# Optimization experiments

Measured on AMD Instinct MI355X. Metric: run time of the kernel, lower is better.

## Reference

```python
import jax, jax.numpy as jnp
import numpy as np
from jax import lax

V, D, H, L, K = 50257, 1024, 2048, 6, 3
B, S = 4, 2048
EPS = 1.1920929e-07  # torch.finfo(float32).eps (torch RMSNorm default eps=None)


def rmsnorm(x, w):
    return x * lax.rsqrt(jnp.mean(x * x, axis=-1, keepdims=True) + EPS) * w


def depthwise_conv(x, w, b):
    # x: (B,S,D), w: (D,1,K) depthwise kernel, padding='same' as in torch Conv1d
    y = lax.conv_general_dilated(x.transpose(0, 2, 1), w, (1,), 'SAME',
                                 dimension_numbers=('NCH', 'OIH', 'NCH'),
                                 feature_group_count=x.shape[-1])
    return y.transpose(0, 2, 1) + b


def mingru(x, h0, wz, bz, wh, bh, wo, bo):
    # minGRU: z=sigmoid(Wz x), h_tilde=Wh x, h_t=(1-z_t)h_{t-1}+z_t h_tilde_t (parallel scan)
    z = jax.nn.sigmoid(jnp.einsum('bsd,hd->bsh', x, wz) + bz)
    htil = jnp.einsum('bsd,hd->bsh', x, wh) + bh
    a, bc = 1.0 - z, z * htil

    def comb(c1, c2):
        a1, b1 = c1
        a2, b2 = c2
        return a1 * a2, a2 * b1 + b2

    A, Bc = lax.associative_scan(comb, (a, bc), axis=1)
    h = A * h0[:, None, :] + Bc                      # (B,S,H)
    out = jnp.einsum('bsh,dh->bsd', h, wo) + bo      # project back to model dim
    return out, h[:, -1]


def setup_inputs():
    key = jax.random.key(0)
    ks = jax.random.split(key, 16)
    sc = 0.02
    p = {}
    p['x'] = jax.random.randint(ks[0], (B, S), 0, V)
    p['h_prev'] = jax.random.normal(ks[1], (B, L, H), jnp.float32)
    p['emb'] = jax.random.normal(ks[2], (V, D), jnp.float32) * sc
    p['conv_dw_w'] = jax.random.normal(ks[3], (L, D, 1, K), jnp.float32) * sc
    p['conv_dw_b'] = jnp.zeros((L, D), jnp.float32)
    p['conv_pw_w'] = jax.random.normal(ks[4], (L, D, D), jnp.float32) * sc
    p['conv_pw_b'] = jnp.zeros((L, D), jnp.float32)
    p['n1_w'] = jnp.ones((L, D), jnp.float32)
    p['wz'] = jax.random.normal(ks[5], (L, H, D), jnp.float32) * sc
    p['bz'] = jnp.zeros((L, H), jnp.float32)
    p['wh'] = jax.random.normal(ks[6], (L, H, D), jnp.float32) * sc
    p['bh'] = jnp.zeros((L, H), jnp.float32)
    p['wo'] = jax.random.normal(ks[7], (L, D, H), jnp.float32) * sc
    p['bo'] = jnp.zeros((L, D), jnp.float32)
    p['n2_w'] = jnp.ones((L, D), jnp.float32)
    p['f1_w'] = jax.random.normal(ks[8], (L, H, D), jnp.float32) * sc
    p['f1_b'] = jnp.zeros((L, H), jnp.float32)
    p['f2_w'] = jax.random.normal(ks[9], (L, D, H), jnp.float32) * sc
    p['f2_b'] = jnp.zeros((L, D), jnp.float32)
    p['norm_w'] = jnp.ones((D,), jnp.float32)
    p['out_w'] = jax.random.normal(ks[10], (H, D), jnp.float32) * sc
    p['out_b'] = jnp.zeros((H,), jnp.float32)
    return p


def reference(x, h_prev, emb, conv_dw_w, conv_dw_b, conv_pw_w, conv_pw_b, n1_w,
              wz, bz, wh, bh, wo, bo, n2_w, f1_w, f1_b, f2_w, f2_b,
              norm_w, out_w, out_b):
    xe = emb[x]                                      # (B,S,D)
    h_next = []
    for l in range(L):
        c = depthwise_conv(xe, conv_dw_w[l], conv_dw_b[l])
        c = jnp.einsum('bsd,ed->bse', c, conv_pw_w[l]) + conv_pw_b[l]  # 1x1 conv
        xe = c + xe
        g, hl = mingru(rmsnorm(xe, n1_w[l]), h_prev[:, l],
                       wz[l], bz[l], wh[l], bh[l], wo[l], bo[l])
        xe = g + xe
        f = rmsnorm(xe, n2_w[l])
        f = jnp.einsum('bsd,hd->bsh', f, f1_w[l]) + f1_b[l]
        f = jax.nn.gelu(f, approximate=False)
        f = jnp.einsum('bsh,dh->bsd', f, f2_w[l]) + f2_b[l]
        xe = f + xe
        h_next.append(hl)
    out = jnp.einsum('bsd,hd->bsh', rmsnorm(xe, norm_w), out_w) + out_b
    return out, jnp.stack(h_next, axis=1)             # (B,S,H), (B,L,H)
```

## Files before the change

kernel.cpp:

```cpp
#include <hip/hip_runtime.h>

typedef __bf16 bf16x8 __attribute__((ext_vector_type(8)));
typedef float f32x4 __attribute__((ext_vector_type(4)));

#define DEVI __device__ __forceinline__

namespace {
constexpr int cB = 4, cS = 2048, cD = 1024, cH = 2048, cL = 6;
constexpr int cM = cB * cS;
constexpr float cEPS = 1.1920929e-07f;
constexpr int NCH = 16, CHS = cS / NCH;
}

DEVI unsigned short f2bf(float f) {
  union { float f; unsigned u; } c; c.f = f;
  const unsigned u = c.u;
  return (unsigned short)((u + 0x7fffu + ((u >> 16) & 1u)) >> 16);
}
DEVI float bf2f(unsigned short h) {
  union { unsigned u; float f; } c; c.u = ((unsigned)h) << 16;
  return c.f;
}

DEVI void gld16(const void* g, void* l) {
  __builtin_amdgcn_global_load_lds(
      (__attribute__((address_space(1))) void*)g,
      (__attribute__((address_space(3))) void*)l, 16, 0, 0);
}

union F4 { float4 v; float a[4]; };

__global__ __launch_bounds__(256) void embed_k(const int* __restrict__ x,
    const float* __restrict__ emb, float* __restrict__ xe) {
  const int bs = blockIdx.x;
  const int idx = x[bs];
  const int t = threadIdx.x;
  *(float4*)&xe[(size_t)bs * cD + t * 4] =
      *(const float4*)&emb[(size_t)idx * cD + t * 4];
}

__global__ __launch_bounds__(256) void dwconv_k(const float* __restrict__ xe,
    const float* __restrict__ w, const float* __restrict__ bias,
    unsigned short* __restrict__ out) {
  const int bs = blockIdx.x;
  const int s = bs & (cS - 1);
  const int t = threadIdx.x;
  const int d = t * 4;
  const size_t base = (size_t)bs * cD + d;
  F4 x0, xm, xp, vb;
  x0.v = *(const float4*)&xe[base];
  xm.v = make_float4(0.f, 0.f, 0.f, 0.f);
  xp.v = make_float4(0.f, 0.f, 0.f, 0.f);
  if (s > 0) xm.v = *(const float4*)&xe[base - cD];
  if (s < cS - 1) xp.v = *(const float4*)&xe[base + cD];
  vb.v = *(const float4*)&bias[d];
  unsigned short o[4];
#pragma unroll
  for (int j = 0; j < 4; ++j) {
    const float w0 = w[(d + j) * 3 + 0];
    const float w1 = w[(d + j) * 3 + 1];
    const float w2 = w[(d + j) * 3 + 2];
    o[j] = f2bf(xm.a[j] * w0 + x0.a[j] * w1 + xp.a[j] * w2 + vb.a[j]);
  }
  *(ushort4*)&out[base] = make_ushort4(o[0], o[1], o[2], o[3]);
}

__global__ __launch_bounds__(256) void rmsnorm_k(const float* __restrict__ x,
    const float* __restrict__ w, unsigned short* __restrict__ o) {
  const int row = blockIdx.x;
  const int t = threadIdx.x;
  const size_t base = (size_t)row * cD + t * 4;
  F4 v; v.v = *(const float4*)&x[base];
  float ss = v.a[0]*v.a[0] + v.a[1]*v.a[1] + v.a[2]*v.a[2] + v.a[3]*v.a[3];
#pragma unroll
  for (int off = 32; off > 0; off >>= 1) ss += __shfl_down(ss, off, 64);
  __shared__ float red[4];
  if ((t & 63) == 0) red[t >> 6] = ss;
  __syncthreads();
  const float scale = rsqrtf((red[0]+red[1]+red[2]+red[3]) * (1.f/cD) + cEPS);
  F4 wv; wv.v = *(const float4*)&w[t * 4];
  *(ushort4*)&o[base] = make_ushort4(
      f2bf(v.a[0]*scale*wv.a[0]), f2bf(v.a[1]*scale*wv.a[1]),
      f2bf(v.a[2]*scale*wv.a[2]), f2bf(v.a[3]*scale*wv.a[3]));
}

__global__ __launch_bounds__(256) void wcvt_k(
    const float* __restrict__ s0, unsigned short* __restrict__ d0,
    const float* __restrict__ s1, unsigned short* __restrict__ d1,
    const float* __restrict__ s2, unsigned short* __restrict__ d2,
    const float* __restrict__ s3, unsigned short* __restrict__ d3,
    const float* __restrict__ s4, unsigned short* __restrict__ d4) {
  constexpr size_t nPW = (size_t)cL * cD * cD;
  constexpr size_t nHD = (size_t)cL * cD * cH;
  constexpr size_t b0 = nPW, b1 = b0 + nHD, b2 = b1 + nHD, b3 = b2 + nHD;
  constexpr size_t total = b3 + (size_t)cH * cD;
  const size_t i = ((size_t)blockIdx.x * 256 + threadIdx.x) * 4;
  if (i >= total) return;
  const float* s; unsigned short* d; size_t off;
  if (i < b0)      { s = s0; d = d0; off = i; }
  else if (i < b1) { s = s1; d = d1; off = i - b0; }
  else if (i < b2) { s = s2; d = d2; off = i - b1; }
  else if (i < b3) { s = s3; d = d3; off = i - b2; }
  else             { s = s4; d = d4; off = i - b3; }
  F4 v; v.v = *(const float4*)&s[off];
  *(ushort4*)&d[off] = make_ushort4(f2bf(v.a[0]), f2bf(v.a[1]),
                                    f2bf(v.a[2]), f2bf(v.a[3]));
}

__global__ __launch_bounds__(256) void cvti2_k(const float* __restrict__ wz,
    const float* __restrict__ wh, unsigned short* __restrict__ d) {
  const size_t i = ((size_t)blockIdx.x * 256 + threadIdx.x) * 4;
  const int l = (int)(i >> 21);
  const int r = (int)((i >> 10) & (cH - 1));
  const int c = (int)(i & (cD - 1));
  F4 a, b; a.v = *(const float4*)&wz[i]; b.v = *(const float4*)&wh[i];
  const size_t dz = (((size_t)l * 2 * cH) + 2 * r) * cD + c;
  *(ushort4*)&d[dz] = make_ushort4(f2bf(a.a[0]), f2bf(a.a[1]),
                                   f2bf(a.a[2]), f2bf(a.a[3]));
  *(ushort4*)&d[dz + cD] = make_ushort4(f2bf(b.a[0]), f2bf(b.a[1]),
                                        f2bf(b.a[2]), f2bf(b.a[3]));
}

__global__ __launch_bounds__(256) void biasi2_k(const float* __restrict__ bz,
    const float* __restrict__ bh, float* __restrict__ d) {
  const int i = blockIdx.x * 256 + threadIdx.x;
  const int l = i >> 11, h = i & (cH - 1);
  d[((size_t)l * 2 * cH) + 2 * h]     = bz[i];
  d[((size_t)l * 2 * cH) + 2 * h + 1] = bh[i];
}

template<int N, int K, int EPI>
__global__ __launch_bounds__(256) void gemm_bt(
    const unsigned short* __restrict__ A, const unsigned short* __restrict__ W,
    const float* __restrict__ bias, float* __restrict__ Cf,
    unsigned short* __restrict__ Cb) {
  __shared__ unsigned short As[128 * 32];
  __shared__ unsigned short Bs[128 * 32];
  const int t = threadIdx.x;
  const int lane = t & 63;
  const int wave = t >> 6;
  const int m0 = blockIdx.x * 128;
  const int n0 = blockIdx.y * 128;
  const int wm = (wave >> 1) * 64;
  const int wn = (wave & 1) * 64;
  const int fr = lane & 15;
  const int fk = ((lane >> 4) * 8) ^ (((lane >> 1) & 3) << 3);

  const int arow = t >> 2;
  const int acol = (((t & 3) ^ ((t >> 3) & 3)) * 8);
  const unsigned short* gA = A + (size_t)(m0 + arow) * K + acol;
  const unsigned short* gB = W + (size_t)(n0 + arow) * K + acol;
  unsigned short* lA = As + wave * 512;
  unsigned short* lB = Bs + wave * 512;

  f32x4 acc[4][4] = {};
  for (int k0 = 0; k0 < K; k0 += 32) {
    gld16(gA + k0, lA);
    gld16(gA + k0 + (size_t)64 * K, lA + 2048);
    gld16(gB + k0, lB);
    gld16(gB + k0 + (size_t)64 * K, lB + 2048);
    __syncthreads();
    bf16x8 fa[4], fb[4];
#pragma unroll
    for (int i = 0; i < 4; ++i) {
      fa[i] = *(const bf16x8*)&As[(wm + i * 16 + fr) * 32 + fk];
      fb[i] = *(const bf16x8*)&Bs[(wn + i * 16 + fr) * 32 + fk];
    }
#pragma unroll
    for (int i = 0; i < 4; ++i)
#pragma unroll
      for (int j = 0; j < 4; ++j)
        acc[i][j] = __builtin_amdgcn_mfma_f32_16x16x32_bf16(
            fa[i], fb[j], acc[i][j], 0, 0, 0);
    __syncthreads();
  }

  const int r0 = m0 + wm + ((lane >> 4) << 2);
  const int c0 = n0 + wn + fr;
#pragma unroll
  for (int i = 0; i < 4; ++i)
#pragma unroll
    for (int j = 0; j < 4; ++j) {
      const int col = c0 + j * 16;
      const float bv = bias[col];
#pragma unroll
      for (int r = 0; r < 4; ++r) {
        const size_t idx = (size_t)(r0 + i * 16 + r) * N + col;
        const float v = acc[i][j][r] + bv;
        if constexpr (EPI == 1) {
          Cf[idx] += v;
        } else {
          Cf[idx] = v;
        }
      }
    }
}

#define RDA(BUF, MH)                                                        \
  _Pragma("unroll") for (int mf = 0; mf < 4; ++mf)                          \
  _Pragma("unroll") for (int kk = 0; kk < 2; ++kk)                          \
      a[mf * 2 + kk] = *(const bf16x8*)&lds[(BUF)*16384 + aB + (MH)*4096 +  \
                                            mf * 1024 + ((kk) ? ck1 : ck0)];

#define RDB0(BUF)                                                           \
  _Pragma("unroll") for (int q = 0; q < 2; ++q)                             \
  _Pragma("unroll") for (int kk = 0; kk < 2; ++kk)                          \
      b[0][q * 2 + kk] = *(const bf16x8*)&lds[(BUF)*16384 + bB + q * 1024 + \
                                              ((kk) ? ck1 : ck0)];

#define RDB1(BUF)                                                           \
  _Pragma("unroll") for (int q = 2; q < 4; ++q)                             \
  _Pragma("unroll") for (int kk = 0; kk < 2; ++kk)                          \
      b[1][(q & 1) * 2 + kk] =                                              \
          *(const bf16x8*)&lds[(BUF)*16384 + bB + q * 1024 +                \
                               ((kk) ? ck1 : ck0)];

#define MMQ(MH, NH)                                                         \
  _Pragma("unroll") for (int mf = 0; mf < 4; ++mf)                          \
  _Pragma("unroll") for (int nf = 0; nf < 2; ++nf)                          \
  _Pragma("unroll") for (int kk = 0; kk < 2; ++kk)                          \
      acc[(MH)*4 + mf][(NH)*2 + nf] = __builtin_amdgcn_mfma_f32_16x16x32_bf16( \
          a[mf * 2 + kk], b[NH][nf * 2 + kk], acc[(MH)*4 + mf][(NH)*2 + nf],  \
          0, 0, 0);

#define PH_SYNC()                                                           \
  __builtin_amdgcn_s_barrier();                                             \
  asm volatile("s_waitcnt lgkmcnt(0)" ::: "memory");                        \
  __builtin_amdgcn_sched_barrier(0);                                        \
  __builtin_amdgcn_s_setprio(1)

#define PH_END()                                                            \
  __builtin_amdgcn_s_setprio(0);                                            \
  __builtin_amdgcn_s_barrier()

#define TILE_PHASES(TI, BUF, OBUF, S1, S2, VM)                              \
  {                                                                         \
    RDA(BUF, 0); RDB0(BUF);                                                 \
    if (S1) { stA((TI) + 1, 1, ldsA(OBUF, 1)); }                            \
    asm volatile("s_waitcnt lgkmcnt(8)" ::: "memory");                      \
    PH_SYNC(); MMQ(0, 0); PH_END();                                         \
    RDB1(BUF);                                                              \
    PH_SYNC(); MMQ(0, 1); PH_END();                                         \
    RDA(BUF, 1);                                                            \
    if (S2) { stB((TI) + 2, 0, ldsB(BUF, 0)); }                             \
    PH_SYNC(); MMQ(1, 1); PH_END();                                         \
    if (S2) { stB((TI) + 2, 1, ldsB(BUF, 1)); stA((TI) + 2, 0, ldsA(BUF, 0)); } \
    if (VM == 6) { asm volatile("s_waitcnt vmcnt(6)" ::: "memory"); }       \
    else         { asm volatile("s_waitcnt vmcnt(0)" ::: "memory"); }       \
    PH_SYNC(); MMQ(1, 0); PH_END();                                         \
  }

template<int N, int K, int EPI>
__global__ __launch_bounds__(512, 2) void gemm8p(
    const unsigned short* __restrict__ A,
    const unsigned short* __restrict__ W0,
    const float* __restrict__ bias0,
    float* __restrict__ Cf, unsigned short* __restrict__ Cb,
    unsigned short* __restrict__ Cb2,
    float* __restrict__ Ac, float* __restrict__ Bc) {
  static_assert(K % 128 == 0, "NT must be even");
  constexpr int NT = K / 64;
  __shared__ unsigned short lds[65536];
  const int t = threadIdx.x;
  const int lane = t & 63;
  const int wave = t >> 6;
  const int wr = wave >> 2;
  const int wc = wave & 3;
  const int m0 = blockIdx.x * 256;
  const int n0 = blockIdx.y * 256;

  const int srow = t >> 3;
  const int scol = (((t & 7) ^ ((t >> 3) & 7)) * 8);
  const unsigned short* gA = A  + (size_t)(m0 + srow) * K + scol;
  const unsigned short* gB = W0 + (size_t)(n0 + srow) * K + scol;
  const int ldsw = wave * 512;

  auto ldsA = [&](int buf, int h) -> unsigned short* {
    return (unsigned short*)&lds[buf * 16384 + h * 8192 + ldsw];
  };
  auto ldsB = [&](int buf, int h) -> unsigned short* {
    return (unsigned short*)&lds[32768 + buf * 16384 + h * 8192 + ldsw];
  };
  auto stA = [&](int tile, int h, unsigned short* dst) {
    const unsigned short* s = gA + (size_t)(h * 128) * K + tile * 64;
    gld16(s, dst);
    gld16(s + (size_t)64 * K, dst + 4096);
  };
  auto stB = [&](int tile, int h, unsigned short* dst) {
    const unsigned short* s = gB + (size_t)(h * 128) * K + tile * 64;
    gld16(s, dst);
    gld16(s + (size_t)64 * K, dst + 4096);
  };

  const int swz = (lane & 7) << 3;
  const int ck0 = (((lane >> 4) * 8)) ^ swz;
  const int ck1 = (32 + ((lane >> 4) * 8)) ^ swz;
  const int aB = wr * 8192 + (lane & 15) * 64;
  const int bB = 32768 + (wc >> 1) * 8192 + (wc & 1) * 4096 + (lane & 15) * 64;

  bf16x8 a[8];
  bf16x8 b[2][4];
  f32x4 acc[8][4] = {};

  stA(0, 0, ldsA(0, 0)); stA(0, 1, ldsA(0, 1));
  stB(0, 0, ldsB(0, 0)); stB(0, 1, ldsB(0, 1));
  stA(1, 0, ldsA(1, 0));
  stB(1, 0, ldsB(1, 0)); stB(1, 1, ldsB(1, 1));
  asm volatile("s_waitcnt vmcnt(6)" ::: "memory");
  __builtin_amdgcn_s_barrier();

  for (int tp = 0; tp < NT / 2 - 1; ++tp) {
    const int t0 = 2 * tp;
    TILE_PHASES(t0, 0, 1, 1, 1, 6);
    TILE_PHASES(t0 + 1, 1, 0, 1, 1, 6);
  }
  TILE_PHASES(NT - 2, 0, 1, 1, 0, 0);
  TILE_PHASES(NT - 1, 1, 0, 0, 0, 0);

  const int r0l = wr * 128 + ((lane >> 4) << 2);
  const int c0l = wc * 64 + (lane & 15);
  if constexpr (EPI == 0) {
    const int r0 = m0 + r0l;
    const int c0 = n0 + c0l;
#pragma unroll
    for (int mfg = 0; mfg < 8; ++mfg)
#pragma unroll
      for (int nfg = 0; nfg < 4; ++nfg) {
        const int col = c0 + nfg * 16;
        const float bv = bias0[col];
#pragma unroll
        for (int r = 0; r < 4; ++r)
          Cf[(size_t)(r0 + mfg * 16 + r) * N + col] = acc[mfg][nfg][r] + bv;
      }
  } else {
    const bool isz = ((lane & 1) == 0);
#pragma unroll
    for (int mfg = 0; mfg < 8; ++mfg)
#pragma unroll
      for (int nfg = 0; nfg < 4; ++nfg) {
        const int col = c0l + nfg * 16;
        const float bv = bias0[n0 + col];
#pragma unroll
        for (int r = 0; r < 4; ++r) {
          const float v = acc[mfg][nfg][r] + bv;
          unsigned short o;
          if constexpr (EPI == 4) {
            o = f2bf(0.5f * v * (1.f + erff(v * 0.70710678118654752f)));
          } else {
            o = isz ? f2bf(1.f / (1.f + __expf(-v))) : f2bf(v);
          }
          const int rr = r0l + mfg * 16 + r;
          lds[rr * 256 + (col ^ (((rr >> 2) & 3) << 4))] = o;
        }
      }
    __syncthreads();
    if constexpr (EPI == 4) {
#pragma unroll
      for (int it = 0; it < 16; ++it) {
        const int flat = it * 512 + t;
        const int row = flat >> 5;
        const int ch = flat & 31;
        const float4 v = *(const float4*)&lds[row * 256 +
                                              ((ch * 8) ^ (((row >> 2) & 3) << 4))];
        *(float4*)&Cb[(size_t)(m0 + row) * N + n0 + ch * 8] = v;
      }
    } else {
#pragma unroll
      for (int it = 0; it < 16; ++it) {
        const int flat = it * 512 + t;
        const int row = flat >> 5;
        const int ch = flat & 31;
        union { float4 v; unsigned u[4]; } q;
        q.v = *(const float4*)&lds[row * 256 +
                                   ((ch * 8) ^ (((row >> 2) & 3) << 4))];
        const ushort4 zz = make_ushort4(q.u[0] & 0xffff, q.u[1] & 0xffff,
                                        q.u[2] & 0xffff, q.u[3] & 0xffff);
        const ushort4 hh = make_ushort4(q.u[0] >> 16, q.u[1] >> 16,
                                        q.u[2] >> 16, q.u[3] >> 16);
        const size_t o = (size_t)(m0 + row) * (N / 2) + (n0 >> 1) + ch * 4;
        *(ushort4*)&Cb[o]  = zz;
        *(ushort4*)&Cb2[o] = hh;
      }
      if (t < 256) {
        const int lc = t >> 7;
        const int lh = t & 127;
        float av = 1.f, bv = 0.f;
        const int s0 = lc * 128;
#pragma unroll 4
        for (int s = 0; s < CHS; ++s) {
          const int sr = s0 + s;
          const int c = (2 * lh) ^ (((sr >> 2) & 3) << 4);
          const unsigned w2 = *(const unsigned*)&lds[sr * 256 + c];
          const float zv = bf2f((unsigned short)(w2 & 0xffff));
          const float hv = bf2f((unsigned short)(w2 >> 16));
          const float aa = 1.f - zv;
          bv = aa * bv + zv * hv;
          av *= aa;
        }
        const int bidx = m0 / cS;
        const int ck = ((m0 & (cS - 1)) >> 7) + lc;
        const int hg = (n0 >> 1) + lh;
        const size_t so = ((size_t)bidx * NCH + ck) * cH + hg;
        Ac[so] = av;
        Bc[so] = bv;
      }
    }
  }
}

__global__ __launch_bounds__(256) void scan23_k(const unsigned short* __restrict__ z,
    unsigned short* __restrict__ ht, const float* __restrict__ Ac,
    const float* __restrict__ Bc, const float* __restrict__ h_prev,
    float* __restrict__ hn, int l) {
  const int tid = blockIdx.x * 256 + threadIdx.x;
  const int hq = (tid & (cH / 4 - 1)) * 4;
  const int ck = (tid / (cH / 4)) & (NCH - 1);
  const int b = tid / ((cH / 4) * NCH);
  const size_t hoff = ((size_t)b * cL + l) * cH + hq;
  F4 h0; h0.v = *(const float4*)&h_prev[hoff];
  float r[4] = {h0.a[0], h0.a[1], h0.a[2], h0.a[3]};
  for (int c = 0; c < ck; ++c) {
    const size_t so = ((size_t)b * NCH + c) * cH + hq;
    F4 av, bv;
    av.v = *(const float4*)&Ac[so];
    bv.v = *(const float4*)&Bc[so];
#pragma unroll
    for (int j = 0; j < 4; ++j) r[j] = av.a[j] * r[j] + bv.a[j];
  }
  const size_t base = ((size_t)b * cS + (size_t)ck * CHS) * cH + hq;
#pragma unroll 4
  for (int s = 0; s < CHS; ++s) {
    const ushort4 zz = *(const ushort4*)&z[base + (size_t)s * cH];
    const ushort4 hh = *(const ushort4*)&ht[base + (size_t)s * cH];
    const float zf[4] = {bf2f(zz.x), bf2f(zz.y), bf2f(zz.z), bf2f(zz.w)};
    const float hf[4] = {bf2f(hh.x), bf2f(hh.y), bf2f(hh.z), bf2f(hh.w)};
#pragma unroll
    for (int j = 0; j < 4; ++j) r[j] = (1.f - zf[j]) * r[j] + zf[j] * hf[j];
    *(ushort4*)&ht[base + (size_t)s * cH] =
        make_ushort4(f2bf(r[0]), f2bf(r[1]), f2bf(r[2]), f2bf(r[3]));
  }
  if (ck == NCH - 1)
    *(float4*)&hn[hoff] = make_float4(r[0], r[1], r[2], r[3]);
}

extern "C" void kernel_launch(void* const* d_in, const int* in_sizes, int n_in,
                              void* d_out, int out_size, void* d_ws, size_t ws_size,
                              hipStream_t stream) {
  (void)in_sizes; (void)n_in; (void)out_size; (void)ws_size;
  const int*   x      = (const int*)d_in[0];
  const float* h_prev = (const float*)d_in[1];
  const float* emb    = (const float*)d_in[2];
  const float* cdw_w  = (const float*)d_in[3];
  const float* cdw_b  = (const float*)d_in[4];
  const float* cpw_w  = (const float*)d_in[5];
  const float* cpw_b  = (const float*)d_in[6];
  const float* n1w    = (const float*)d_in[7];
  const float* wzp    = (const float*)d_in[8];
  const float* bzp    = (const float*)d_in[9];
  const float* whp    = (const float*)d_in[10];
  const float* bhp    = (const float*)d_in[11];
  const float* wop    = (const float*)d_in[12];
  const float* bop    = (const float*)d_in[13];
  const float* n2w    = (const float*)d_in[14];
  const float* f1wp   = (const float*)d_in[15];
  const float* f1bp   = (const float*)d_in[16];
  const float* f2wp   = (const float*)d_in[17];
  const float* f2bp   = (const float*)d_in[18];
  const float* nw     = (const float*)d_in[19];
  const float* owp    = (const float*)d_in[20];
  const float* obp    = (const float*)d_in[21];

  float* out_main = (float*)d_out;
  float* out_hn   = out_main + (size_t)cM * cH;

  char* p = (char*)d_ws;
  auto alloc = [&](size_t bytes) {
    char* r = p; p += (bytes + 255) & ~(size_t)255; return r;
  };
  float*          xe = (float*)alloc((size_t)cM * cD * 4);
  unsigned short* xn = (unsigned short*)alloc((size_t)cM * cD * 2);
  unsigned short* zb = (unsigned short*)alloc((size_t)cM * cH * 2);
  unsigned short* hb = (unsigned short*)alloc((size_t)cM * cH * 2);
  float* Ac = (float*)alloc((size_t)cB * NCH * cH * 4);
  float* Bc = (float*)alloc((size_t)cB * NCH * cH * 4);
  unsigned short* w_pw = (unsigned short*)alloc((size_t)cL * cD * cD * 2);
  unsigned short* w_zh = (unsigned short*)alloc((size_t)cL * 2 * cH * cD * 2);
  float*          bzh  = (float*)alloc((size_t)cL * 2 * cH * 4);
  unsigned short* w_o  = (unsigned short*)alloc((size_t)cL * cD * cH * 2);
  unsigned short* w_f1 = (unsigned short*)alloc((size_t)cL * cH * cD * 2);
  unsigned short* w_f2 = (unsigned short*)alloc((size_t)cL * cD * cH * 2);
  unsigned short* w_ow = (unsigned short*)alloc((size_t)cH * cD * 2);

  {
    constexpr size_t total = (size_t)cL * cD * cD + 3 * (size_t)cL * cD * cH +
                             (size_t)cH * cD;
    wcvt_k<<<dim3((unsigned)(total / 1024)), 256, 0, stream>>>(
        cpw_w, w_pw, wop, w_o, f1wp, w_f1, f2wp, w_f2, owp, w_ow);
    cvti2_k<<<dim3(cL * cH * cD / 1024), 256, 0, stream>>>(wzp, whp, w_zh);
    biasi2_k<<<dim3(cL * cH / 256), 256, 0, stream>>>(bzp, bhp, bzh);
  }

  embed_k<<<cM, 256, 0, stream>>>(x, emb, xe);

  for (int l = 0; l < cL; ++l) {
    const size_t oDD = (size_t)l * cD * cD, oHD = (size_t)l * cH * cD;

    dwconv_k<<<cM, 256, 0, stream>>>(xe, cdw_w + (size_t)l * cD * 3,
                                     cdw_b + (size_t)l * cD, xn);
    gemm_bt<cD, cD, 1><<<dim3(cM / 128, cD / 128), 256, 0, stream>>>(
        xn, w_pw + oDD, cpw_b + (size_t)l * cD, xe, nullptr);

    rmsnorm_k<<<cM, 256, 0, stream>>>(xe, n1w + (size_t)l * cD, xn);
    gemm8p<2 * cH, cD, 6><<<dim3(cM / 256, 2 * cH / 256), 512, 0, stream>>>(
        xn, w_zh + (size_t)l * 2 * cH * cD, bzh + (size_t)l * 2 * cH,
        nullptr, zb, hb, Ac, Bc);
    scan23_k<<<cB * NCH * (cH / 4) / 256, 256, 0, stream>>>(zb, hb, Ac, Bc,
                                                            h_prev, out_hn, l);
    gemm_bt<cD, cH, 1><<<dim3(cM / 128, cD / 128), 256, 0, stream>>>(
        hb, w_o + oHD, bop + (size_t)l * cD, xe, nullptr);

    rmsnorm_k<<<cM, 256, 0, stream>>>(xe, n2w + (size_t)l * cD, xn);
    gemm8p<cH, cD, 4><<<dim3(cM / 256, cH / 256), 512, 0, stream>>>(
        xn, w_f1 + oHD, f1bp + (size_t)l * cH, nullptr, zb, nullptr,
        nullptr, nullptr);
    gemm_bt<cD, cH, 1><<<dim3(cM / 128, cD / 128), 256, 0, stream>>>(
        zb, w_f2 + oHD, f2bp + (size_t)l * cD, xe, nullptr);
  }

  rmsnorm_k<<<cM, 256, 0, stream>>>(xe, nw, xn);
  gemm8p<cH, cD, 0><<<dim3(cM / 256, cH / 256), 512, 0, stream>>>(
      xn, w_ow, obp, out_main, nullptr, nullptr, nullptr, nullptr);
}
```

Measured before the change: 2.317 ms.

## Replace simple residual GEMMs with pipelined 256x128 eight-wave MFMA kernel

The three N=1024 residual-add GEMMs (pointwise conv, minGRU output projection, FFN down projection) move from a single-buffered 128x128 kernel with two barriers per K step to a new 512-thread 256x128 kernel. The new kernel uses double-buffered LDS with async prefetch two tiles ahead and phased barriers with s_setprio, mirroring the existing gemm8p schedule. The goal is to hide global load latency and raise MFMA utilisation. In exchange it uses more LDS per block (96KB) and yields half as many blocks (256) per GEMM, which could underfill the GPU.

```diff
diff --git a/kernel.cpp b/kernel.cpp
--- a/kernel.cpp
+++ b/kernel.cpp
@@ -129,100 +129,6 @@
   d[((size_t)l * 2 * cH) + 2 * h + 1] = bh[i];
 }
 
-template<int N, int K, int EPI>
-__global__ __launch_bounds__(256) void gemm_bt(
-    const unsigned short* __restrict__ A, const unsigned short* __restrict__ W,
-    const float* __restrict__ bias, float* __restrict__ Cf,
-    unsigned short* __restrict__ Cb) {
-  __shared__ unsigned short As[128 * 32];
-  __shared__ unsigned short Bs[128 * 32];
-  const int t = threadIdx.x;
-  const int lane = t & 63;
-  const int wave = t >> 6;
-  const int m0 = blockIdx.x * 128;
-  const int n0 = blockIdx.y * 128;
-  const int wm = (wave >> 1) * 64;
-  const int wn = (wave & 1) * 64;
-  const int fr = lane & 15;
-  const int fk = ((lane >> 4) * 8) ^ (((lane >> 1) & 3) << 3);
-
-  const int arow = t >> 2;
-  const int acol = (((t & 3) ^ ((t >> 3) & 3)) * 8);
-  const unsigned short* gA = A + (size_t)(m0 + arow) * K + acol;
-  const unsigned short* gB = W + (size_t)(n0 + arow) * K + acol;
-  unsigned short* lA = As + wave * 512;
-  unsigned short* lB = Bs + wave * 512;
-
-  f32x4 acc[4][4] = {};
-  for (int k0 = 0; k0 < K; k0 += 32) {
-    gld16(gA + k0, lA);
-    gld16(gA + k0 + (size_t)64 * K, lA + 2048);
-    gld16(gB + k0, lB);
-    gld16(gB + k0 + (size_t)64 * K, lB + 2048);
-    __syncthreads();
-    bf16x8 fa[4], fb[4];
-#pragma unroll
-    for (int i = 0; i < 4; ++i) {
-      fa[i] = *(const bf16x8*)&As[(wm + i * 16 + fr) * 32 + fk];
-      fb[i] = *(const bf16x8*)&Bs[(wn + i * 16 + fr) * 32 + fk];
-    }
-#pragma unroll
-    for (int i = 0; i < 4; ++i)
-#pragma unroll
-      for (int j = 0; j < 4; ++j)
-        acc[i][j] = __builtin_amdgcn_mfma_f32_16x16x32_bf16(
-            fa[i], fb[j], acc[i][j], 0, 0, 0);
-    __syncthreads();
-  }
-
-  const int r0 = m0 + wm + ((lane >> 4) << 2);
-  const int c0 = n0 + wn + fr;
-#pragma unroll
-  for (int i = 0; i < 4; ++i)
-#pragma unroll
-    for (int j = 0; j < 4; ++j) {
-      const int col = c0 + j * 16;
-      const float bv = bias[col];
-#pragma unroll
-      for (int r = 0; r < 4; ++r) {
-        const size_t idx = (size_t)(r0 + i * 16 + r) * N + col;
-        const float v = acc[i][j][r] + bv;
-        if constexpr (EPI == 1) {
-          Cf[idx] += v;
-        } else {
-          Cf[idx] = v;
-        }
-      }
-    }
-}
-
-#define RDA(BUF, MH)                                                        \
-  _Pragma("unroll") for (int mf = 0; mf < 4; ++mf)                          \
-  _Pragma("unroll") for (int kk = 0; kk < 2; ++kk)                          \
-      a[mf * 2 + kk] = *(const bf16x8*)&lds[(BUF)*16384 + aB + (MH)*4096 +  \
-                                            mf * 1024 + ((kk) ? ck1 : ck0)];
-
-#define RDB0(BUF)                                                           \
-  _Pragma("unroll") for (int q = 0; q < 2; ++q)                             \
-  _Pragma("unroll") for (int kk = 0; kk < 2; ++kk)                          \
-      b[0][q * 2 + kk] = *(const bf16x8*)&lds[(BUF)*16384 + bB + q * 1024 + \
-                                              ((kk) ? ck1 : ck0)];
-
-#define RDB1(BUF)                                                           \
-  _Pragma("unroll") for (int q = 2; q < 4; ++q)                             \
-  _Pragma("unroll") for (int kk = 0; kk < 2; ++kk)                          \
-      b[1][(q & 1) * 2 + kk] =                                              \
-          *(const bf16x8*)&lds[(BUF)*16384 + bB + q * 1024 +                \
-                               ((kk) ? ck1 : ck0)];
-
-#define MMQ(MH, NH)                                                         \
-  _Pragma("unroll") for (int mf = 0; mf < 4; ++mf)                          \
-  _Pragma("unroll") for (int nf = 0; nf < 2; ++nf)                          \
-  _Pragma("unroll") for (int kk = 0; kk < 2; ++kk)                          \
-      acc[(MH)*4 + mf][(NH)*2 + nf] = __builtin_amdgcn_mfma_f32_16x16x32_bf16( \
-          a[mf * 2 + kk], b[NH][nf * 2 + kk], acc[(MH)*4 + mf][(NH)*2 + nf],  \
-          0, 0, 0);
-
 #define PH_SYNC()                                                           \
   __builtin_amdgcn_s_barrier();                                             \
   asm volatile("s_waitcnt lgkmcnt(0)" ::: "memory");                        \
@@ -232,6 +138,144 @@
 #define PH_END()                                                            \
   __builtin_amdgcn_s_setprio(0);                                            \
   __builtin_amdgcn_s_barrier()
+
+#define RDA_N(BUF, MH)                                                      \
+  _Pragma("unroll") for (int mf = 0; mf < 4; ++mf)                          \
+  _Pragma("unroll") for (int kk = 0; kk < 2; ++kk)                          \
+      a[mf * 2 + kk] = *(const bf16x8*)&lds[(BUF)*16384 + aB + (MH)*4096 +  \
+                                            mf * 1024 + ((kk) ? ck1 : ck0)];
+
+#define RDB_N(BUF, NH)                                                      \
+  _Pragma("unroll") for (int kk = 0; kk < 2; ++kk)                          \
+      b[NH][kk] = *(const bf16x8*)&lds[32768 + (BUF)*8192 + bB +            \
+                                       (NH)*1024 + ((kk) ? ck1 : ck0)];
+
+#define MMQ_N(MH, NH)                                                       \
+  _Pragma("unroll") for (int mf = 0; mf < 4; ++mf)                          \
+  _Pragma("unroll") for (int kk = 0; kk < 2; ++kk)                          \
+      acc[(MH)*4 + mf][NH] = __builtin_amdgcn_mfma_f32_16x16x32_bf16(       \
+          a[mf * 2 + kk], b[NH][kk], acc[(MH)*4 + mf][NH], 0, 0, 0);
+
+#define TILE_N(TI, BUF, OBUF, S1, S2, VM)                                   \
+  {                                                                         \
+    RDA_N(BUF, 0); RDB_N(BUF, 0);                                           \
+    if (S1) { stA((TI) + 1, 1, ldsA(OBUF, 1)); }                            \
+    PH_SYNC(); MMQ_N(0, 0); PH_END();                                       \
+    RDB_N(BUF, 1);                                                          \
+    PH_SYNC(); MMQ_N(0, 1); PH_END();                                       \
+    RDA_N(BUF, 1);                                                          \
+    if (S2) { stB((TI) + 2, ldsB(BUF)); }                                   \
+    PH_SYNC(); MMQ_N(1, 1); PH_END();                                       \
+    if (S2) { stA((TI) + 2, 0, ldsA(BUF, 0)); }                             \
+    if (VM == 4) { asm volatile("s_waitcnt vmcnt(4)" ::: "memory"); }       \
+    else         { asm volatile("s_waitcnt vmcnt(0)" ::: "memory"); }       \
+    PH_SYNC(); MMQ_N(1, 0); PH_END();                                       \
+  }
+
+template<int N, int K>
+__global__ __launch_bounds__(512, 2) void gemm8n(
+    const unsigned short* __restrict__ A,
+    const unsigned short* __restrict__ W,
+    const float* __restrict__ bias, float* __restrict__ Cf) {
+  static_assert(K % 128 == 0, "NT must be even");
+  constexpr int NT = K / 64;
+  __shared__ unsigned short lds[49152];
+  const int t = threadIdx.x;
+  const int lane = t & 63;
+  const int wave = t >> 6;
+  const int wr = wave >> 2;
+  const int wc = wave & 3;
+  const int m0 = blockIdx.x * 256;
+  const int n0 = blockIdx.y * 128;
+
+  const int srow = t >> 3;
+  const int scol = (((t & 7) ^ ((t >> 3) & 7)) * 8);
+  const unsigned short* gA = A + (size_t)(m0 + srow) * K + scol;
+  const unsigned short* gB = W + (size_t)(n0 + srow) * K + scol;
+  const int ldsw = wave * 512;
+
+  auto ldsA = [&](int buf, int h) -> unsigned short* {
+    return (unsigned short*)&lds[buf * 16384 + h * 8192 + ldsw];
+  };
+  auto ldsB = [&](int buf) -> unsigned short* {
+    return (unsigned short*)&lds[32768 + buf * 8192 + ldsw];
+  };
+  auto stA = [&](int tile, int h, unsigned short* dst) {
+    const unsigned short* s = gA + (size_t)(h * 128) * K + tile * 64;
+    gld16(s, dst);
+    gld16(s + (size_t)64 * K, dst + 4096);
+  };
+  auto stB = [&](int tile, unsigned short* dst) {
+    const unsigned short* s = gB + (size_t)tile * 64;
+    gld16(s, dst);
+    gld16(s + (size_t)64 * K, dst + 4096);
+  };
+
+  const int swz = (lane & 7) << 3;
+  const int ck0 = ((lane >> 4) * 8) ^ swz;
+  const int ck1 = (32 + (lane >> 4) * 8) ^ swz;
+  const int aB = wr * 8192 + (lane & 15) * 64;
+  const int bB = wc * 2048 + (lane & 15) * 64;
+
+  bf16x8 a[8];
+  bf16x8 b[2][2];
+  f32x4 acc[8][2] = {};
+
+  stA(0, 0, ldsA(0, 0)); stA(0, 1, ldsA(0, 1));
+  stB(0, ldsB(0));
+  stA(1, 0, ldsA(1, 0));
+  stB(1, ldsB(1));
+  asm volatile("s_waitcnt vmcnt(4)" ::: "memory");
+  __builtin_amdgcn_s_barrier();
+
+  for (int tp = 0; tp < NT / 2 - 1; ++tp) {
+    const int t0 = 2 * tp;
+    TILE_N(t0, 0, 1, 1, 1, 4);
+    TILE_N(t0 + 1, 1, 0, 1, 1, 4);
+  }
+  TILE_N(NT - 2, 0, 1, 1, 0, 0);
+  TILE_N(NT - 1, 1, 0, 0, 0, 0);
+
+  const int r0 = m0 + wr * 128 + ((lane >> 4) << 2);
+  const int c0 = n0 + wc * 32 + (lane & 15);
+#pragma unroll
+  for (int mfg = 0; mfg < 8; ++mfg)
+#pragma unroll
+    for (int nfg = 0; nfg < 2; ++nfg) {
+      const int col = c0 + nfg * 16;
+      const float bv = bias[col];
+#pragma unroll
+      for (int r = 0; r < 4; ++r)
+        Cf[(size_t)(r0 + mfg * 16 + r) * N + col] += acc[mfg][nfg][r] + bv;
+    }
+}
+
+#define RDA(BUF, MH)                                                        \
+  _Pragma("unroll") for (int mf = 0; mf < 4; ++mf)                          \
+  _Pragma("unroll") for (int kk = 0; kk < 2; ++kk)                          \
+      a[mf * 2 + kk] = *(const bf16x8*)&lds[(BUF)*16384 + aB + (MH)*4096 +  \
+                                            mf * 1024 + ((kk) ? ck1 : ck0)];
+
+#define RDB0(BUF)                                                           \
+  _Pragma("unroll") for (int q = 0; q < 2; ++q)                             \
+  _Pragma("unroll") for (int kk = 0; kk < 2; ++kk)                          \
+      b[0][q * 2 + kk] = *(const bf16x8*)&lds[(BUF)*16384 + bB + q * 1024 + \
+                                              ((kk) ? ck1 : ck0)];
+
+#define RDB1(BUF)                                                           \
+  _Pragma("unroll") for (int q = 2; q < 4; ++q)                             \
+  _Pragma("unroll") for (int kk = 0; kk < 2; ++kk)                          \
+      b[1][(q & 1) * 2 + kk] =                                              \
+          *(const bf16x8*)&lds[(BUF)*16384 + bB + q * 1024 +                \
+                               ((kk) ? ck1 : ck0)];
+
+#define MMQ(MH, NH)                                                         \
+  _Pragma("unroll") for (int mf = 0; mf < 4; ++mf)                          \
+  _Pragma("unroll") for (int nf = 0; nf < 2; ++nf)                          \
+  _Pragma("unroll") for (int kk = 0; kk < 2; ++kk)                          \
+      acc[(MH)*4 + mf][(NH)*2 + nf] = __builtin_amdgcn_mfma_f32_16x16x32_bf16( \
+          a[mf * 2 + kk], b[NH][nf * 2 + kk], acc[(MH)*4 + mf][(NH)*2 + nf],  \
+          0, 0, 0);
 
 #define TILE_PHASES(TI, BUF, OBUF, S1, S2, VM)                              \
   {                                                                         \
@@ -507,8 +551,8 @@
 
     dwconv_k<<<cM, 256, 0, stream>>>(xe, cdw_w + (size_t)l * cD * 3,
                                      cdw_b + (size_t)l * cD, xn);
-    gemm_bt<cD, cD, 1><<<dim3(cM / 128, cD / 128), 256, 0, stream>>>(
-        xn, w_pw + oDD, cpw_b + (size_t)l * cD, xe, nullptr);
+    gemm8n<cD, cD><<<dim3(cM / 256, cD / 128), 512, 0, stream>>>(
+        xn, w_pw + oDD, cpw_b + (size_t)l * cD, xe);
 
     rmsnorm_k<<<cM, 256, 0, stream>>>(xe, n1w + (size_t)l * cD, xn);
     gemm8p<2 * cH, cD, 6><<<dim3(cM / 256, 2 * cH / 256), 512, 0, stream>>>(
@@ -516,15 +560,15 @@
         nullptr, zb, hb, Ac, Bc);
     scan23_k<<<cB * NCH * (cH / 4) / 256, 256, 0, stream>>>(zb, hb, Ac, Bc,
                                                             h_prev, out_hn, l);
-    gemm_bt<cD, cH, 1><<<dim3(cM / 128, cD / 128), 256, 0, stream>>>(
-        hb, w_o + oHD, bop + (size_t)l * cD, xe, nullptr);
+    gemm8n<cD, cH><<<dim3(cM / 256, cD / 128), 512, 0, stream>>>(
+        hb, w_o + oHD, bop + (size_t)l * cD, xe);
 
     rmsnorm_k<<<cM, 256, 0, stream>>>(xe, n2w + (size_t)l * cD, xn);
     gemm8p<cH, cD, 4><<<dim3(cM / 256, cH / 256), 512, 0, stream>>>(
         xn, w_f1 + oHD, f1bp + (size_t)l * cH, nullptr, zb, nullptr,
         nullptr, nullptr);
-    gemm_bt<cD, cH, 1><<<dim3(cM / 128, cD / 128), 256, 0, stream>>>(
-        zb, w_f2 + oHD, f2bp + (size_t)l * cD, xe, nullptr);
+    gemm8n<cD, cH><<<dim3(cM / 256, cD / 128), 512, 0, stream>>>(
+        zb, w_f2 + oHD, f2bp + (size_t)l * cD, xe);
   }
 
   rmsnorm_k<<<cM, 256, 0, stream>>>(xe, nw, xn);
```

Result: faster. 1.995 ms (median of 2 runs) (-13.9%).
